# Kernel tuning notes

Measured on AMD Instinct MI355X. Metric: run time of the kernel, lower is better.

Reference implementation:

```python
import jax, jax.numpy as jnp
import numpy as np

B, S, D, H = 2, 2048, 1024, 16
HD = D // H

def setup_inputs() -> dict:
    key = jax.random.key(0)
    ks = jax.random.split(key, 5)
    scale = 1.0 / np.sqrt(D)
    x = jax.random.normal(ks[0], (B, S, D), dtype=jnp.float32)
    W_qkv = jax.random.normal(ks[1], (D, 3 * D), dtype=jnp.float32) * scale
    b_qkv = jnp.zeros((3 * D,), dtype=jnp.float32)
    W_proj = jax.random.normal(ks[2], (D, D), dtype=jnp.float32) * scale
    b_proj = jnp.zeros((D,), dtype=jnp.float32)
    return {"x": x, "W_qkv": W_qkv, "b_qkv": b_qkv, "W_proj": W_proj, "b_proj": b_proj}

def reference(x, W_qkv, b_qkv, W_proj, b_proj):
    # qkv projection: [B,S,3D]
    qkv = jnp.einsum('bsd,df->bsf', x, W_qkv) + b_qkv
    q, k, v = jnp.split(qkv, 3, axis=-1)
    # reshape to heads: [B,H,S,hd]
    q = q.reshape(B, S, H, HD).transpose(0, 2, 1, 3)
    k = k.reshape(B, S, H, HD).transpose(0, 2, 1, 3)
    v = v.reshape(B, S, H, HD).transpose(0, 2, 1, 3)
    scores = jnp.einsum('bhqd,bhkd->bhqk', q, k) / jnp.sqrt(jnp.float32(HD))
    attn = jax.nn.softmax(scores, axis=-1)
    out = jnp.einsum('bhqk,bhkd->bhqd', attn, v)
    out = out.transpose(0, 2, 1, 3).reshape(B, S, D)
    return jnp.einsum('bsd,df->bsf', out, W_proj) + b_proj
```

## Files before the change

### kernel.cpp

```cpp
#include <hip/hip_runtime.h>

#define BATCH 2
#define SLEN 2048
#define DMODEL 1024
#define NHEAD 16
#define HDIM 64
#define MROWS (BATCH * SLEN)

typedef __attribute__((ext_vector_type(8))) short bf16x8;
typedef __attribute__((ext_vector_type(4))) short bf16x4;
typedef __attribute__((ext_vector_type(4))) float f32x4;
typedef __attribute__((ext_vector_type(8))) _Float16 f16x8;
typedef __attribute__((ext_vector_type(4))) _Float16 f16x4;

__device__ inline short f2bf(float x) {
    union { float f; unsigned u; } v; v.f = x;
    unsigned r = (v.u + 0x7FFFu + ((v.u >> 16) & 1u)) >> 16;
    return (short)r;
}
__device__ inline float bf2f(short h) {
    union { unsigned u; float f; } v; v.u = ((unsigned)(unsigned short)h) << 16;
    return v.f;
}
__device__ inline unsigned fbits(float x) {
    union { float f; unsigned u; } v; v.f = x; return v.u;
}
__device__ inline float hw_exp2(float x) {
#if __has_builtin(__builtin_amdgcn_exp2f)
    return __builtin_amdgcn_exp2f(x);
#else
    float r;
    asm("v_exp_f32 %0, %1" : "=v"(r) : "v"(x));
    return r;
#endif
}

__global__ __launch_bounds__(256) void cast_f16(
    const float* __restrict__ in, _Float16* __restrict__ out, int n4)
{
    int i = blockIdx.x * 256 + threadIdx.x;
    if (i >= n4) return;
    float4 f = ((const float4*)in)[i];
    f16x4 h;
    h[0] = (_Float16)f.x; h[1] = (_Float16)f.y;
    h[2] = (_Float16)f.z; h[3] = (_Float16)f.w;
    ((f16x4*)out)[i] = h;
}

__global__ __launch_bounds__(256) void transpose_f16(
    const float* __restrict__ in, _Float16* __restrict__ outT, int K, int N)
{
    __shared__ float T[64][68];
    const int tid = threadIdx.x;
    const int n0 = blockIdx.x * 64, k0 = blockIdx.y * 64;
#pragma unroll
    for (int i = 0; i < 4; i++) {
        int idx = tid + i * 256;
        int r = idx >> 4, c4 = idx & 15;
        *(float4*)&T[r][c4 * 4] = *(const float4*)&in[(size_t)(k0 + r) * N + n0 + c4 * 4];
    }
    __syncthreads();
#pragma unroll
    for (int i = 0; i < 4; i++) {
        int idx = tid + i * 256;
        int n = idx >> 4, kg = idx & 15;
        f16x4 h;
#pragma unroll
        for (int j = 0; j < 4; j++)
            h[j] = (_Float16)T[kg * 4 + j][n];
        *(f16x4*)&outT[(size_t)(n0 + n) * K + k0 + kg * 4] = h;
    }
}

__global__ __launch_bounds__(256) void transpose_v(
    const short* __restrict__ qkv, short* __restrict__ vT)
{
    __shared__ short T[64 * 68];
    const int tid = threadIdx.x;
    const int bid = blockIdx.x;
    const int st = bid & 31, h = (bid >> 5) & 15, b = bid >> 9;
    const int s0 = st * 64;
    const short* src = qkv + (size_t)b * SLEN * (3 * DMODEL) + 2 * DMODEL + h * HDIM;

    const int srow = tid >> 3, sc8 = tid & 7;
#pragma unroll
    for (int it = 0; it < 2; it++) {
        int s = srow + it * 32;
        *(bf16x8*)&T[s * 68 + sc8 * 8] =
            *(const bf16x8*)&src[(size_t)(s0 + s) * (3 * DMODEL) + sc8 * 8];
    }
    __syncthreads();

    const int d = tid >> 2, sq = tid & 3;
    short* dst = vT + ((size_t)(b * NHEAD + h) * HDIM + d) * SLEN + s0 + sq * 16;
    bf16x8 o0, o1;
#pragma unroll
    for (int j = 0; j < 8; j++) {
        o0[j] = T[(sq * 16 + j) * 68 + d];
        o1[j] = T[(sq * 16 + 8 + j) * 68 + d];
    }
    *(bf16x8*)&dst[0] = o0;
    *(bf16x8*)&dst[8] = o1;
}

#define GSTR 40

template<int OUT_BF16>
__global__ __launch_bounds__(256) void gemm_f16(
    const _Float16* __restrict__ A, const _Float16* __restrict__ Bw,
    const float* __restrict__ bias, void* __restrict__ Cout,
    int M, int N, int K)
{
    __shared__ _Float16 As[128 * GSTR], Bs[128 * GSTR];

    const int tid  = threadIdx.x;
    const int wave = tid >> 6, lane = tid & 63;
    const int quad = lane >> 4, lr = lane & 15;
    const int wm = (wave >> 1) * 64, wn = (wave & 1) * 64;
    const int row0 = blockIdx.y * 128, col0 = blockIdx.x * 128;

    f32x4 acc[4][4];
#pragma unroll
    for (int i = 0; i < 4; i++)
#pragma unroll
        for (int j = 0; j < 4; j++) acc[i][j] = (f32x4){0.f, 0.f, 0.f, 0.f};

    const int sr = tid >> 2, sc = tid & 3;

    for (int k0 = 0; k0 < K; k0 += 32) {
        __syncthreads();
#pragma unroll
        for (int i = 0; i < 2; i++) {
            int rr = sr + i * 64;
            size_t ga = (size_t)(row0 + rr) * K + k0 + sc * 8;
            size_t gb = (size_t)(col0 + rr) * K + k0 + sc * 8;
            int ls = rr * GSTR + sc * 8;
            *(f16x8*)&As[ls] = *(const f16x8*)&A[ga];
            *(f16x8*)&Bs[ls] = *(const f16x8*)&Bw[gb];
        }
        __syncthreads();

        f16x8 af[4];
#pragma unroll
        for (int mt = 0; mt < 4; mt++)
            af[mt] = *(const f16x8*)&As[(wm + mt * 16 + lr) * GSTR + quad * 8];
#pragma unroll
        for (int nt = 0; nt < 4; nt++) {
            f16x8 b = *(const f16x8*)&Bs[(wn + nt * 16 + lr) * GSTR + quad * 8];
#pragma unroll
            for (int mt = 0; mt < 4; mt++)
                acc[mt][nt] = __builtin_amdgcn_mfma_f32_16x16x32_f16(af[mt], b, acc[mt][nt], 0, 0, 0);
        }
    }

#pragma unroll
    for (int mt = 0; mt < 4; mt++) {
#pragma unroll
        for (int nt = 0; nt < 4; nt++) {
            int col = col0 + wn + nt * 16 + lr;
            float bv = bias[col];
#pragma unroll
            for (int r = 0; r < 4; r++) {
                int row = row0 + wm + mt * 16 + quad * 4 + r;
                float v = acc[mt][nt][r] + bv;
                if (OUT_BF16)
                    ((short*)Cout)[(size_t)row * N + col] = f2bf(v);
                else
                    ((float*)Cout)[(size_t)row * N + col] = v;
            }
        }
    }
}

#define ASTR 76
#define NT   (SLEN / 64)
#define QK_SCALE_LOG2E 0.1803368801111244f

__global__ __launch_bounds__(256) void attn_mfma(
    const short* __restrict__ qkv, const short* __restrict__ vT,
    _Float16* __restrict__ attn)
{
    __shared__ short Ks[2][64 * ASTR];
    __shared__ short Vt[2][64 * ASTR];

    const int tid  = threadIdx.x;
    const int lane = tid & 63;
    const int wave = tid >> 6;
    const int quad = lane >> 4;
    const int lr   = lane & 15;
    const int wq0  = wave * 32;

    const int bid = blockIdx.x;
    const int qt = bid & 15;
    const int h  = (bid >> 4) & 15;
    const int b  = bid >> 8;
    const int q0 = qt * 128;

    const short* qbase = qkv + (size_t)b * SLEN * (3 * DMODEL) + h * HDIM;
    const short* kbase = qbase + DMODEL;
    const short* vtbase = vT + (size_t)(b * NHEAD + h) * HDIM * SLEN;

    bf16x4 qf[2][4];
#pragma unroll
    for (int qs = 0; qs < 2; qs++)
#pragma unroll
        for (int ds = 0; ds < 4; ds++) {
            bf16x4 q = *(const bf16x4*)&qbase[(size_t)(q0 + wq0 + qs * 16 + lr) * (3 * DMODEL) + ds * 16 + quad * 4];
#pragma unroll
            for (int j = 0; j < 4; j++)
                q[j] = f2bf(bf2f(q[j]) * QK_SCALE_LOG2E);
            qf[qs][ds] = q;
        }

    bf16x4 ones;
#pragma unroll
    for (int j = 0; j < 4; j++) ones[j] = (short)0x3F80;

    f32x4 oacc[2][4];
#pragma unroll
    for (int qs = 0; qs < 2; qs++)
#pragma unroll
        for (int t = 0; t < 4; t++) oacc[qs][t] = (f32x4){0.f, 0.f, 0.f, 0.f};
    f32x4 sacc[2] = {{0.f, 0.f, 0.f, 0.f}, {0.f, 0.f, 0.f, 0.f}};

    const int srow = tid >> 3, sc8 = tid & 7;

    const short* kp0 = kbase + (size_t)srow * (3 * DMODEL) + sc8 * 8;
    const short* kp1 = kp0 + 32 * (3 * DMODEL);
    const short* vp0 = vtbase + (size_t)srow * SLEN + sc8 * 8;
    const short* vp1 = vp0 + 32 * SLEN;

    bf16x8 kpre[2], vpre[2];
    kpre[0] = *(const bf16x8*)kp0; kpre[1] = *(const bf16x8*)kp1;
    vpre[0] = *(const bf16x8*)vp0; vpre[1] = *(const bf16x8*)vp1;
    kp0 += 64 * (3 * DMODEL); kp1 += 64 * (3 * DMODEL);
    vp0 += 64; vp1 += 64;

    for (int kt = 0; kt < NT; kt++) {
        const int cur = kt & 1;
        short* ks = Ks[cur];
        short* vt = Vt[cur];

        *(bf16x8*)&ks[srow * ASTR + sc8 * 8] = kpre[0];
        *(bf16x8*)&ks[(srow + 32) * ASTR + sc8 * 8] = kpre[1];
        *(bf16x8*)&vt[srow * ASTR + sc8 * 8] = vpre[0];
        *(bf16x8*)&vt[(srow + 32) * ASTR + sc8 * 8] = vpre[1];

        if (kt + 1 < NT) {
            kpre[0] = *(const bf16x8*)kp0; kpre[1] = *(const bf16x8*)kp1;
            vpre[0] = *(const bf16x8*)vp0; vpre[1] = *(const bf16x8*)vp1;
            kp0 += 64 * (3 * DMODEL); kp1 += 64 * (3 * DMODEL);
            vp0 += 64; vp1 += 64;
        }

        __syncthreads();

#pragma unroll
        for (int ct = 0; ct < 4; ct++) {
            bf16x4 kf[4];
#pragma unroll
            for (int ds = 0; ds < 4; ds++)
                kf[ds] = *(const bf16x4*)&ks[(ct * 16 + lr) * ASTR + ds * 16 + quad * 4];

            f32x4 st0 = {0.f, 0.f, 0.f, 0.f}, st1 = {0.f, 0.f, 0.f, 0.f};
#pragma unroll
            for (int ds = 0; ds < 4; ds++) {
                st0 = __builtin_amdgcn_mfma_f32_16x16x16bf16_1k(kf[ds], qf[0][ds], st0, 0, 0, 0);
                st1 = __builtin_amdgcn_mfma_f32_16x16x16bf16_1k(kf[ds], qf[1][ds], st1, 0, 0, 0);
            }

            float p0[4], p1[4];
#pragma unroll
            for (int r = 0; r < 4; r++) { p0[r] = hw_exp2(st0[r]); p1[r] = hw_exp2(st1[r]); }
            union { uint2 u; bf16x4 v; } pk0, pk1;
            pk0.u.x = __builtin_amdgcn_perm(fbits(p0[1]), fbits(p0[0]), 0x07060302u);
            pk0.u.y = __builtin_amdgcn_perm(fbits(p0[3]), fbits(p0[2]), 0x07060302u);
            pk1.u.x = __builtin_amdgcn_perm(fbits(p1[1]), fbits(p1[0]), 0x07060302u);
            pk1.u.y = __builtin_amdgcn_perm(fbits(p1[3]), fbits(p1[2]), 0x07060302u);
            bf16x4 pf0 = pk0.v, pf1 = pk1.v;

            sacc[0] = __builtin_amdgcn_mfma_f32_16x16x16bf16_1k(ones, pf0, sacc[0], 0, 0, 0);
            sacc[1] = __builtin_amdgcn_mfma_f32_16x16x16bf16_1k(ones, pf1, sacc[1], 0, 0, 0);
#pragma unroll
            for (int dt = 0; dt < 4; dt++) {
                bf16x4 vf = *(const bf16x4*)&vt[(dt * 16 + lr) * ASTR + ct * 16 + quad * 4];
                oacc[0][dt] = __builtin_amdgcn_mfma_f32_16x16x16bf16_1k(vf, pf0, oacc[0][dt], 0, 0, 0);
                oacc[1][dt] = __builtin_amdgcn_mfma_f32_16x16x16bf16_1k(vf, pf1, oacc[1][dt], 0, 0, 0);
            }
        }
    }

#pragma unroll
    for (int qs = 0; qs < 2; qs++) {
        const float inv = 1.0f / sacc[qs][0];
        const int row = b * SLEN + q0 + wq0 + qs * 16 + lr;
#pragma unroll
        for (int dt = 0; dt < 4; dt++) {
            f16x4 h4;
#pragma unroll
            for (int r = 0; r < 4; r++)
                h4[r] = (_Float16)(oacc[qs][dt][r] * inv);
            int col = h * HDIM + dt * 16 + quad * 4;
            *(f16x4*)&attn[(size_t)row * DMODEL + col] = h4;
        }
    }
}

extern "C" void kernel_launch(void* const* d_in, const int* in_sizes, int n_in,
                              void* d_out, int out_size, void* d_ws, size_t ws_size,
                              hipStream_t stream) {
    (void)in_sizes; (void)n_in; (void)out_size; (void)ws_size;
    const float* x     = (const float*)d_in[0];
    const float* Wqkv  = (const float*)d_in[1];
    const float* bqkv  = (const float*)d_in[2];
    const float* Wproj = (const float*)d_in[3];
    const float* bproj = (const float*)d_in[4];
    float* out = (float*)d_out;

    short* qkv = (short*)d_ws;
    _Float16* xf = (_Float16*)(qkv + (size_t)MROWS * 3 * DMODEL);
    _Float16* wq = xf + (size_t)MROWS * DMODEL;
    _Float16* wp = wq + (size_t)3 * DMODEL * DMODEL;
    short* vT = (short*)(wp + (size_t)DMODEL * DMODEL);
    _Float16* attnb = (_Float16*)(vT + (size_t)MROWS * DMODEL);

    cast_f16<<<dim3(MROWS * DMODEL / 4 / 256), 256, 0, stream>>>(x, xf, MROWS * DMODEL / 4);
    transpose_f16<<<dim3(3 * DMODEL / 64, DMODEL / 64), 256, 0, stream>>>(Wqkv, wq, DMODEL, 3 * DMODEL);
    transpose_f16<<<dim3(DMODEL / 64, DMODEL / 64), 256, 0, stream>>>(Wproj, wp, DMODEL, DMODEL);

    gemm_f16<1><<<dim3(3 * DMODEL / 128, MROWS / 128), 256, 0, stream>>>(
        xf, wq, bqkv, (void*)qkv, MROWS, 3 * DMODEL, DMODEL);

    transpose_v<<<dim3(BATCH * NHEAD * (SLEN / 64)), 256, 0, stream>>>(qkv, vT);

    attn_mfma<<<dim3(BATCH * NHEAD * (SLEN / 128)), 256, 0, stream>>>(qkv, vT, attnb);

    gemm_f16<0><<<dim3(DMODEL / 128, MROWS / 128), 256, 0, stream>>>(
        attnb, wp, bproj, (void*)out, MROWS, DMODEL, DMODEL);
}
```

Measured before the change: 221.1 us.

## Halve attention query tile and use 16x16x32 bf16 MFMA for QK^T

Each attention workgroup now handles 64 query rows instead of 128, so each wave owns 16 queries and the grid doubles to 1024 blocks. The QK^T product switches from four 16x16x16 MFMAs to two 16x16x32 MFMAs using 8-wide bf16 fragments. The LDS row stride also drops from 76 to 72 shorts, and the exp2 helper now always uses inline v_exp_f32 asm. The aim is more parallelism and fewer, wider matrix instructions. The cost is that every K/V tile is loaded and staged once per 64 queries, doubling K/V traffic, with a possible change in LDS bank conflicts.

Result: slower. 226.4 us (+2.4%).

```diff
diff --git a/kernel.cpp b/kernel.cpp
--- a/kernel.cpp
+++ b/kernel.cpp
@@ -26,13 +26,9 @@
     union { float f; unsigned u; } v; v.f = x; return v.u;
 }
 __device__ inline float hw_exp2(float x) {
-#if __has_builtin(__builtin_amdgcn_exp2f)
-    return __builtin_amdgcn_exp2f(x);
-#else
     float r;
     asm("v_exp_f32 %0, %1" : "=v"(r) : "v"(x));
     return r;
-#endif
 }
 
 __global__ __launch_bounds__(256) void cast_f16(
@@ -172,7 +168,7 @@
     }
 }
 
-#define ASTR 76
+#define ASTR 72
 #define NT   (SLEN / 64)
 #define QK_SCALE_LOG2E 0.1803368801111244f
 
@@ -188,40 +184,36 @@
     const int wave = tid >> 6;
     const int quad = lane >> 4;
     const int lr   = lane & 15;
-    const int wq0  = wave * 32;
+    const int wq0  = wave * 16;
 
     const int bid = blockIdx.x;
-    const int qt = bid & 15;
-    const int h  = (bid >> 4) & 15;
-    const int b  = bid >> 8;
-    const int q0 = qt * 128;
+    const int qt = bid & 31;
+    const int h  = (bid >> 5) & 15;
+    const int b  = bid >> 9;
+    const int q0 = qt * 64;
 
     const short* qbase = qkv + (size_t)b * SLEN * (3 * DMODEL) + h * HDIM;
     const short* kbase = qbase + DMODEL;
     const short* vtbase = vT + (size_t)(b * NHEAD + h) * HDIM * SLEN;
 
-    bf16x4 qf[2][4];
-#pragma unroll
-    for (int qs = 0; qs < 2; qs++)
-#pragma unroll
-        for (int ds = 0; ds < 4; ds++) {
-            bf16x4 q = *(const bf16x4*)&qbase[(size_t)(q0 + wq0 + qs * 16 + lr) * (3 * DMODEL) + ds * 16 + quad * 4];
-#pragma unroll
-            for (int j = 0; j < 4; j++)
-                q[j] = f2bf(bf2f(q[j]) * QK_SCALE_LOG2E);
-            qf[qs][ds] = q;
-        }
+    bf16x8 qf[2];
+#pragma unroll
+    for (int ds2 = 0; ds2 < 2; ds2++) {
+        bf16x8 q = *(const bf16x8*)&qbase[(size_t)(q0 + wq0 + lr) * (3 * DMODEL) + ds2 * 32 + quad * 8];
+#pragma unroll
+        for (int j = 0; j < 8; j++)
+            q[j] = f2bf(bf2f(q[j]) * QK_SCALE_LOG2E);
+        qf[ds2] = q;
+    }
 
     bf16x4 ones;
 #pragma unroll
     for (int j = 0; j < 4; j++) ones[j] = (short)0x3F80;
 
-    f32x4 oacc[2][4];
-#pragma unroll
-    for (int qs = 0; qs < 2; qs++)
-#pragma unroll
-        for (int t = 0; t < 4; t++) oacc[qs][t] = (f32x4){0.f, 0.f, 0.f, 0.f};
-    f32x4 sacc[2] = {{0.f, 0.f, 0.f, 0.f}, {0.f, 0.f, 0.f, 0.f}};
+    f32x4 oacc[4];
+#pragma unroll
+    for (int t = 0; t < 4; t++) oacc[t] = (f32x4){0.f, 0.f, 0.f, 0.f};
+    f32x4 sacc = {0.f, 0.f, 0.f, 0.f};
 
     const int srow = tid >> 3, sc8 = tid & 7;
 
@@ -257,49 +249,39 @@
 
 #pragma unroll
         for (int ct = 0; ct < 4; ct++) {
-            bf16x4 kf[4];
-#pragma unroll
-            for (int ds = 0; ds < 4; ds++)
-                kf[ds] = *(const bf16x4*)&ks[(ct * 16 + lr) * ASTR + ds * 16 + quad * 4];
-
-            f32x4 st0 = {0.f, 0.f, 0.f, 0.f}, st1 = {0.f, 0.f, 0.f, 0.f};
-#pragma unroll
-            for (int ds = 0; ds < 4; ds++) {
-                st0 = __builtin_amdgcn_mfma_f32_16x16x16bf16_1k(kf[ds], qf[0][ds], st0, 0, 0, 0);
-                st1 = __builtin_amdgcn_mfma_f32_16x16x16bf16_1k(kf[ds], qf[1][ds], st1, 0, 0, 0);
-            }
-
-            float p0[4], p1[4];
-#pragma unroll
-            for (int r = 0; r < 4; r++) { p0[r] = hw_exp2(st0[r]); p1[r] = hw_exp2(st1[r]); }
-            union { uint2 u; bf16x4 v; } pk0, pk1;
+            bf16x8 kf0 = *(const bf16x8*)&ks[(ct * 16 + lr) * ASTR + quad * 8];
+            bf16x8 kf1 = *(const bf16x8*)&ks[(ct * 16 + lr) * ASTR + 32 + quad * 8];
+
+            f32x4 st = {0.f, 0.f, 0.f, 0.f};
+            st = __builtin_amdgcn_mfma_f32_16x16x32_bf16(kf0, qf[0], st, 0, 0, 0);
+            st = __builtin_amdgcn_mfma_f32_16x16x32_bf16(kf1, qf[1], st, 0, 0, 0);
+
+            float p0[4];
+#pragma unroll
+            for (int r = 0; r < 4; r++) p0[r] = hw_exp2(st[r]);
+            union { uint2 u; bf16x4 v; } pk0;
             pk0.u.x = __builtin_amdgcn_perm(fbits(p0[1]), fbits(p0[0]), 0x07060302u);
             pk0.u.y = __builtin_amdgcn_perm(fbits(p0[3]), fbits(p0[2]), 0x07060302u);
-            pk1.u.x = __builtin_amdgcn_perm(fbits(p1[1]), fbits(p1[0]), 0x07060302u);
-            pk1.u.y = __builtin_amdgcn_perm(fbits(p1[3]), fbits(p1[2]), 0x07060302u);
-            bf16x4 pf0 = pk0.v, pf1 = pk1.v;
-
-            sacc[0] = __builtin_amdgcn_mfma_f32_16x16x16bf16_1k(ones, pf0, sacc[0], 0, 0, 0);
-            sacc[1] = __builtin_amdgcn_mfma_f32_16x16x16bf16_1k(ones, pf1, sacc[1], 0, 0, 0);
+            bf16x4 pf0 = pk0.v;
+
+            sacc = __builtin_amdgcn_mfma_f32_16x16x16bf16_1k(ones, pf0, sacc, 0, 0, 0);
 #pragma unroll
             for (int dt = 0; dt < 4; dt++) {
                 bf16x4 vf = *(const bf16x4*)&vt[(dt * 16 + lr) * ASTR + ct * 16 + quad * 4];
-                oacc[0][dt] = __builtin_amdgcn_mfma_f32_16x16x16bf16_1k(vf, pf0, oacc[0][dt], 0, 0, 0);
-                oacc[1][dt] = __builtin_amdgcn_mfma_f32_16x16x16bf16_1k(vf, pf1, oacc[1][dt], 0, 0, 0);
+                oacc[dt] = __builtin_amdgcn_mfma_f32_16x16x16bf16_1k(vf, pf0, oacc[dt], 0, 0, 0);
             }
         }
     }
 
-#pragma unroll
-    for (int qs = 0; qs < 2; qs++) {
-        const float inv = 1.0f / sacc[qs][0];
-        const int row = b * SLEN + q0 + wq0 + qs * 16 + lr;
+    {
+        const float inv = 1.0f / sacc[0];
+        const int row = b * SLEN + q0 + wq0 + lr;
 #pragma unroll
         for (int dt = 0; dt < 4; dt++) {
             f16x4 h4;
 #pragma unroll
             for (int r = 0; r < 4; r++)
-                h4[r] = (_Float16)(oacc[qs][dt][r] * inv);
+                h4[r] = (_Float16)(oacc[dt][r] * inv);
             int col = h * HDIM + dt * 16 + quad * 4;
             *(f16x4*)&attn[(size_t)row * DMODEL + col] = h4;
         }
@@ -333,7 +315,7 @@
 
     transpose_v<<<dim3(BATCH * NHEAD * (SLEN / 64)), 256, 0, stream>>>(qkv, vT);
 
-    attn_mfma<<<dim3(BATCH * NHEAD * (SLEN / 128)), 256, 0, stream>>>(qkv, vT, attnb);
+    attn_mfma<<<dim3(BATCH * NHEAD * (SLEN / 64)), 256, 0, stream>>>(qkv, vT, attnb);
 
     gemm_f16<0><<<dim3(DMODEL / 128, MROWS / 128), 256, 0, stream>>>(
         attnb, wp, bproj, (void*)out, MROWS, DMODEL, DMODEL);
```
